# Performance work log

Hardware: AMD Instinct MI355X
Metric: run time of the kernel (lower is better)

Reference implementation:

```python
import jax, jax.numpy as jnp
import numpy as np

B, S, D = 1, 2048, 2048
H, HD = 16, 128  # n_heads, head_dim
ROPE_BASE = 100000.0


def setup_inputs() -> dict:
    key = jax.random.key(0)
    k0, k1, k2 = jax.random.split(key, 3)
    x = jax.random.normal(k0, (B, S, D), jnp.float32)
    # real RoPE table: (seq_len, head_dim//2, 2) holding (cos, sin)
    inv_freq = 1.0 / (ROPE_BASE ** (np.arange(0, HD, 2, dtype=np.float64) / HD))
    t = np.arange(S, dtype=np.float64)[:, None] * inv_freq[None, :]
    freqs_cis = jnp.asarray(np.stack([np.cos(t), np.sin(t)], axis=-1), jnp.float32)
    input_pos = jnp.arange(S, dtype=jnp.int32)
    Wqkv = jax.random.normal(k1, (D, 3 * D), jnp.float32) * (D ** -0.5)
    bqkv = jnp.zeros((3 * D,), jnp.float32)
    Wdense = jax.random.normal(k2, (D, D), jnp.float32) * (D ** -0.5)
    bdense = jnp.zeros((D,), jnp.float32)
    return {"x": x, "freqs_cis": freqs_cis, "input_pos": input_pos,
            "Wqkv": Wqkv, "bqkv": bqkv, "Wdense": Wdense, "bdense": bdense}


def apply_rotary_emb(x, freqs_cis):
    # x: [B, S, H, HD]; freqs_cis: [S, HD//2, 2]
    xs = x.reshape(*x.shape[:-1], -1, 2)  # [B,S,H,HD/2,2]
    fc = freqs_cis.reshape(1, xs.shape[1], 1, xs.shape[3], 2)
    out = jnp.stack([
        xs[..., 0] * fc[..., 0] - xs[..., 1] * fc[..., 1],
        xs[..., 1] * fc[..., 0] + xs[..., 0] * fc[..., 1],
    ], axis=-1)
    return out.reshape(x.shape).astype(x.dtype)


def reference(x, freqs_cis, input_pos, Wqkv, bqkv, Wdense, bdense):
    b, s, d = x.shape
    qkv = x @ Wqkv + bqkv                      # fused QKV projection
    q, k, v = jnp.split(qkv, 3, axis=-1)
    q = q.reshape(b, s, H, HD)
    k = k.reshape(b, s, H, HD)
    v = v.reshape(b, s, H, HD)
    q = apply_rotary_emb(q, freqs_cis)
    k = apply_rotary_emb(k, freqs_cis)
    # KV-cache update (cache batch = 1, max_seq = context_length)
    k_cache = jnp.zeros((1, S, H, HD), jnp.float32)
    v_cache = jnp.zeros((1, S, H, HD), jnp.float32)
    k_full = k_cache.at[:, input_pos].set(k)
    v_full = v_cache.at[:, input_pos].set(v)
    # causal SDPA in [B, H, S, HD] layout
    qh = q.transpose(0, 2, 1, 3)
    kh = k_full.transpose(0, 2, 1, 3)
    vh = v_full.transpose(0, 2, 1, 3)
    scale = HD ** -0.5
    scores = jnp.einsum('bhqd,bhkd->bhqk', qh, kh) * scale  # [B,H,S,S]
    causal = jnp.tril(jnp.ones((s, S), dtype=bool))
    scores = jnp.where(causal, scores, jnp.finfo(scores.dtype).min)
    attn = jax.nn.softmax(scores, axis=-1)
    ctx = jnp.einsum('bhqk,bhkd->bhqd', attn, vh)
    ctx = ctx.transpose(0, 2, 1, 3).reshape(b, s, d)
    return ctx @ Wdense + bdense
```

## Files before the change

kernel.cpp:

```cpp
#include <hip/hip_runtime.h>

#define S 2048
#define D 2048
#define H 16
#define HD 128
#define N3 6144

typedef __attribute__((ext_vector_type(8))) _Float16 f16x8;
typedef __attribute__((ext_vector_type(4))) float f32x4;
typedef unsigned short ushort_t;
typedef unsigned int uint_t;

__device__ __forceinline__ ushort_t f16_rne(float f) {
    _Float16 h = (_Float16)f;
    return __builtin_bit_cast(ushort_t, h);
}
__device__ __forceinline__ float f16_f32(ushort_t u) {
    return (float)__builtin_bit_cast(_Float16, u);
}

__global__ __launch_bounds__(256) void convert_f16_kernel(
    const float* __restrict__ in, ushort_t* __restrict__ hi)
{
    const int i = blockIdx.x * 256 + threadIdx.x;
    float4 v = ((const float4*)in)[i];
    ((ushort4*)hi)[i] = make_ushort4(f16_rne(v.x), f16_rne(v.y),
                                     f16_rne(v.z), f16_rne(v.w));
}

__global__ __launch_bounds__(256) void convert_t_kernel(
    const float* __restrict__ in, ushort_t* __restrict__ hi,
    int Kdim, int Ndim)
{
    __shared__ float tile[32][33];
    const int k0 = blockIdx.x * 32, n0 = blockIdx.y * 32;
    const int tx = threadIdx.x & 31, ty = threadIdx.x >> 5;
    #pragma unroll
    for (int r = 0; r < 4; r++)
        tile[ty + r * 8][tx] = in[(size_t)(k0 + ty + r * 8) * Ndim + n0 + tx];
    __syncthreads();
    const int n  = threadIdx.x >> 3;
    const int kc = (threadIdx.x & 7) * 4;
    const float v0 = tile[kc + 0][n], v1 = tile[kc + 1][n];
    const float v2 = tile[kc + 2][n], v3 = tile[kc + 3][n];
    const size_t off = (size_t)(n0 + n) * Kdim + k0 + kc;
    *(ushort4*)&hi[off] = make_ushort4(f16_rne(v0), f16_rne(v1),
                                       f16_rne(v2), f16_rne(v3));
}

__device__ __forceinline__ void gload16(const ushort_t* g, ushort_t* l) {
    __builtin_amdgcn_global_load_lds(
        (const __attribute__((address_space(1))) unsigned int*)g,
        (__attribute__((address_space(3))) unsigned int*)l, 16, 0, 0);
}

__device__ __forceinline__ void vwait8() { asm volatile("s_waitcnt vmcnt(8)" ::: "memory"); }
__device__ __forceinline__ void vwait4() { asm volatile("s_waitcnt vmcnt(4)" ::: "memory"); }
__device__ __forceinline__ void vwait0() { asm volatile("s_waitcnt vmcnt(0)" ::: "memory"); }
__device__ __forceinline__ void lwait0() { asm volatile("s_waitcnt lgkmcnt(0)" ::: "memory"); }

#define QNT 32

__device__ __forceinline__ void mm_core_8ph(
    const ushort_t* __restrict__ At, const ushort_t* __restrict__ Bt,
    ushort_t* lds, const int t, f32x4 (&acc)[4][4])
{
    const int w = t >> 6, lane = t & 63;
    const int lr = lane & 15, quad = lane >> 4;
    const int wm = (w & 1) * 64;
    const int wn = (w >> 1) * 64;

    const int srow = lane >> 2;
    const int scol = (lane & 3) * 8;
    const size_t goff0 = (size_t)(w * 16 + srow) * D + scol;
    const size_t goff1 = goff0 + (size_t)64 * D;
    const int ldst0 = w * 512;
    const int ldst1 = 2048 + w * 512;

    auto stage = [&](int j, int Tt) {
        const ushort_t* gb = (j & 1) ? Bt : At;
        const size_t off = (size_t)Tt * 64 + (j >> 1) * 32;
        ushort_t* dst = lds + (Tt & 1) * 16384 + j * 4096;
        gload16(gb + goff0 + off, dst + ldst0);
        gload16(gb + goff1 + off, dst + ldst1);
    };

    const int aro = (wm + lr) * 32 + quad * 8;
    const int bro = 4096 + (wn + lr) * 32 + quad * 8;

    stage(0, 0); stage(1, 0); stage(2, 0); stage(3, 0);
    stage(0, 1); stage(1, 1);
    vwait4();
    __builtin_amdgcn_sched_barrier(0);
    __builtin_amdgcn_s_barrier();

    f16x8 af[4], bf[4];

#define PH(kk, DOSTAGE, ST, WAITN)                                         \
    {                                                                      \
        const ushort_t* base = lds + (T & 1) * 16384 + (kk) * 8192;        \
        _Pragma("unroll")                                                  \
        for (int i = 0; i < 4; i++)                                        \
            af[i] = *(const f16x8*)&base[aro + i * 512];                   \
        _Pragma("unroll")                                                  \
        for (int n = 0; n < 4; n++)                                        \
            bf[n] = *(const f16x8*)&base[bro + n * 512];                   \
        if (DOSTAGE) {                                                     \
            stage((kk) ? 0 : 2, ST);                                       \
            stage((kk) ? 1 : 3, ST);                                       \
        }                                                                  \
        __builtin_amdgcn_s_barrier();                                      \
        lwait0();                                                          \
        __builtin_amdgcn_sched_barrier(0);                                 \
        __builtin_amdgcn_s_setprio(1);                                     \
        _Pragma("unroll")                                                  \
        for (int i = 0; i < 4; i++)                                        \
            _Pragma("unroll")                                              \
            for (int n = 0; n < 4; n++)                                    \
                acc[i][n] = __builtin_amdgcn_mfma_f32_16x16x32_f16(        \
                    af[i], bf[n], acc[i][n], 0, 0, 0);                     \
        __builtin_amdgcn_s_setprio(0);                                     \
        WAITN;                                                             \
        __builtin_amdgcn_s_barrier();                                      \
    }

    for (int T = 0; T < QNT - 2; T++) {
        PH(0, true, T + 1, vwait8());
        PH(1, true, T + 2, vwait8());
    }
    {
        const int T = QNT - 2;
        PH(0, true,  T + 1, vwait8());
        PH(1, false, 0,     vwait4());
    }
    {
        const int T = QNT - 1;
        PH(0, false, 0, vwait0());
        PH(1, false, 0, );
    }
#undef PH
}

__global__ __launch_bounds__(256, 2) void gemm_qkv_mfma(
    const ushort_t* __restrict__ xh,
    const ushort_t* __restrict__ Wth,
    const float* __restrict__ bias, const float* __restrict__ freqs,
    const int* __restrict__ input_pos,
    ushort_t* __restrict__ qhg, ushort_t* __restrict__ khg,
    ushort_t* __restrict__ vhg)
{
    __shared__ ushort_t lds[32768];
    const int t = threadIdx.x;
    const int col0 = blockIdx.x * 128;
    const int row0 = blockIdx.y * 128;

    f32x4 acc[4][4] = {};
    mm_core_8ph(xh + (size_t)row0 * D, Wth + (size_t)col0 * D, lds, t, acc);

    const int lane = t & 63;
    const int quad = lane >> 4;
    const int lr   = lane & 15;
    const int w = t >> 6;
    const int wm = (w & 1) * 64;
    const int wn = (w >> 1) * 64;

    const int which = col0 >> 11;
    const int hh = (col0 & 2047) >> 7;

    if (which == 2) {
        ushort_t* vh_b = vhg + (size_t)hh * HD * S;
        #pragma unroll
        for (int nt = 0; nt < 4; nt++) {
            const int d = wn + nt * 16 + lr;
            const float bsc = bias[col0 + d];
            #pragma unroll
            for (int mt = 0; mt < 4; mt++) {
                #pragma unroll
                for (int reg = 0; reg < 4; reg++) {
                    const int m = row0 + wm + mt * 16 + quad * 4 + reg;
                    const float v = acc[mt][nt][reg] + bsc;
                    vh_b[(size_t)d * S + input_pos[m]] = f16_rne(v);
                }
            }
        }
    } else {
        ushort_t* oh_b = ((which == 0) ? qhg : khg) + (size_t)hh * S * HD;
        #pragma unroll
        for (int nt = 0; nt < 4; nt++) {
            const int d = wn + nt * 16 + lr;
            const float bsc = bias[col0 + d];
            #pragma unroll
            for (int mt = 0; mt < 4; mt++) {
                #pragma unroll
                for (int reg = 0; reg < 4; reg++) {
                    const int m = row0 + wm + mt * 16 + quad * 4 + reg;
                    const float v = acc[mt][nt][reg] + bsc;
                    const float* fc = &freqs[((size_t)m * 64 + (d >> 1)) * 2];
                    const float cc = fc[0], ss = fc[1];
                    const float p = __shfl_xor(v, 1);
                    const float o = (d & 1) ? (v * cc + p * ss) : (v * cc - p * ss);
                    const ushort_t hv = f16_rne(o);
                    const int hp = __shfl_xor((int)hv, 1);
                    if (!(d & 1)) {
                        const int srowg = (which == 0) ? m : input_pos[m];
                        *(uint_t*)&oh_b[(size_t)srowg * HD + d] =
                            (uint_t)hv | ((uint_t)hp << 16);
                    }
                }
            }
        }
    }
}

__global__ __launch_bounds__(256, 2) void gemm_dense_mfma(
    const ushort_t* __restrict__ Ah,
    const ushort_t* __restrict__ Wth,
    const float* __restrict__ bias, float* __restrict__ out)
{
    __shared__ ushort_t lds[32768];
    const int t = threadIdx.x;
    const int col0 = blockIdx.x * 128;
    const int row0 = blockIdx.y * 128;

    f32x4 acc[4][4] = {};
    mm_core_8ph(Ah + (size_t)row0 * D, Wth + (size_t)col0 * D, lds, t, acc);

    const int lane = t & 63;
    const int quad = lane >> 4;
    const int lr   = lane & 15;
    const int w = t >> 6;
    const int wm = (w & 1) * 64;
    const int wn = (w >> 1) * 64;

    #pragma unroll
    for (int nt = 0; nt < 4; nt++) {
        const int n = col0 + wn + nt * 16 + lr;
        const float bsc = bias[n];
        #pragma unroll
        for (int mt = 0; mt < 4; mt++) {
            #pragma unroll
            for (int reg = 0; reg < 4; reg++) {
                const int m = row0 + wm + mt * 16 + quad * 4 + reg;
                const float o = acc[mt][nt][reg] + bsc;
                const float po = __shfl_xor(o, 1);
                if (!(n & 1))
                    *(float2*)&out[(size_t)m * D + n] = make_float2(o, po);
            }
        }
    }
}

__global__ __launch_bounds__(256, 2) void attn_mfma_kernel(
    const ushort_t* __restrict__ qhg, const ushort_t* __restrict__ khg,
    const ushort_t* __restrict__ vhg,
    float* __restrict__ Opart, float* __restrict__ MLpart)
{
    __shared__ ushort_t Khs[2][4096];
    __shared__ ushort_t Vhs[2][4096];
    __shared__ ushort_t Ps[64 * 32];

    const int bi   = blockIdx.x;
    const int h    = (bi & 7) + 8 * ((bi >> 3) & 1);
    const int half = (bi >> 4) & 1;
    const int qi   = bi >> 5;
    const int r = (h & 8) ? qi : (31 - qi);
    const int q0 = r * 64;
    const int nhalf = r + 1;
    const int kt0 = half * nhalf;
    const int kt1 = kt0 + nhalf;
    const int t = threadIdx.x;
    const int w = t >> 6, lane = t & 63;
    const int lr = lane & 15, quad = lane >> 4;

    const size_t qrow = (size_t)h * S + q0 + w * 16 + lr;
    f16x8 qf[4];
    #pragma unroll
    for (int ks = 0; ks < 4; ks++)
        qf[ks] = *(const f16x8*)&qhg[qrow * HD + ks * 32 + quad * 8];

    const ushort_t* kh_b = khg + (size_t)h * S * HD;
    const ushort_t* vh_b = vhg + (size_t)h * HD * S;

    const int keyq = lane >> 2;
    const int sub  = lane & 3;

    auto stage = [&](int kt, int buf) {
        const int k0 = kt * 32;
        #pragma unroll
        for (int hf = 0; hf < 2; hf++) {
            const size_t ksrc = (size_t)(k0 + hf * 16 + keyq) * HD + w * 32 + sub * 8;
            gload16(kh_b + ksrc, &Khs[buf][w * 1024 + hf * 512]);
            const int dim = w * 32 + hf * 16 + keyq;
            const size_t vsrc = (size_t)dim * S + k0 + sub * 8;
            gload16(vh_b + vsrc, &Vhs[buf][(w * 32 + hf * 16) * 32]);
        }
    };

    f32x4 O[8] = {};
    f32x4 Ol = {0.f, 0.f, 0.f, 0.f};
    float mrow[4];
    #pragma unroll
    for (int rr = 0; rr < 4; rr++) mrow[rr] = -1e30f;

    f16x8 onesv;
    #pragma unroll
    for (int i = 0; i < 8; i++) onesv[i] = (_Float16)1.0f;

    const float kSc = 0.08838834764831845f * 1.4426950408889634f;

    stage(kt0, 0);

    for (int kt = kt0; kt < kt1; kt++) {
        const int k0 = kt * 32;
        const int cur = (kt - kt0) & 1;
        __syncthreads();

        if (kt + 1 < kt1) stage(kt + 1, cur ^ 1);

        f32x4 sa[2];
        #pragma unroll
        for (int nt = 0; nt < 2; nt++) {
            f32x4 s = {0.f, 0.f, 0.f, 0.f};
            #pragma unroll
            for (int ks = 0; ks < 4; ks++) {
                f16x8 kf = *(const f16x8*)&Khs[cur][ks * 1024 + (nt * 16 + lr) * 32 + quad * 8];
                s = __builtin_amdgcn_mfma_f32_16x16x32_f16(qf[ks], kf, s, 0, 0, 0);
            }
            sa[nt] = s;
        }

        const int rowbase = q0 + w * 16 + quad * 4;
        const bool need_mask = (k0 + 31) > (q0 + w * 16);
        float alpha[4], pv0[4], pv1[4];
        #pragma unroll
        for (int rr = 0; rr < 4; rr++) {
            float z0 = sa[0][rr] * kSc;
            float z1 = sa[1][rr] * kSc;
            if (need_mask) {
                const int rowg = rowbase + rr;
                if (k0 + lr > rowg)      z0 = -1e30f;
                if (k0 + 16 + lr > rowg) z1 = -1e30f;
            }
            float rm = fmaxf(z0, z1);
            #pragma unroll
            for (int off = 1; off < 16; off <<= 1)
                rm = fmaxf(rm, __shfl_xor(rm, off));
            const float nm = fmaxf(mrow[rr], rm);
            alpha[rr] = exp2f(mrow[rr] - nm);
            pv0[rr] = exp2f(z0 - nm);
            pv1[rr] = exp2f(z1 - nm);
            mrow[rr] = nm;
        }

        #pragma unroll
        for (int rr = 0; rr < 4; rr++) {
            const int prow = (w * 16 + quad * 4 + rr) * 32;
            Ps[prow + lr]      = f16_rne(pv0[rr]);
            Ps[prow + 16 + lr] = f16_rne(pv1[rr]);
        }

        #pragma unroll
        for (int nt = 0; nt < 8; nt++)
            #pragma unroll
            for (int rr = 0; rr < 4; rr++)
                O[nt][rr] *= alpha[rr];
        #pragma unroll
        for (int rr = 0; rr < 4; rr++)
            Ol[rr] *= alpha[rr];
        const f16x8 pf = *(const f16x8*)&Ps[(w * 16 + lr) * 32 + quad * 8];
        #pragma unroll
        for (int nt = 0; nt < 8; nt++) {
            f16x8 vf = *(const f16x8*)&Vhs[cur][(nt * 16 + lr) * 32 + quad * 8];
            O[nt] = __builtin_amdgcn_mfma_f32_16x16x32_f16(pf, vf, O[nt], 0, 0, 0);
        }
        Ol = __builtin_amdgcn_mfma_f32_16x16x32_f16(pf, onesv, Ol, 0, 0, 0);
    }

    float* Ob = Opart + (size_t)bi * 64 * 128;
    #pragma unroll
    for (int rr = 0; rr < 4; rr++) {
        const int row = w * 16 + quad * 4 + rr;
        #pragma unroll
        for (int nt = 0; nt < 8; nt++)
            Ob[(size_t)row * 128 + nt * 16 + lr] = O[nt][rr];
        if (lr == 0) {
            MLpart[(size_t)bi * 128 + row * 2 + 0] = mrow[rr];
            MLpart[(size_t)bi * 128 + row * 2 + 1] = Ol[rr];
        }
    }
}

__global__ __launch_bounds__(128) void attn_combine_kernel(
    const float* __restrict__ Opart, const float* __restrict__ MLpart,
    ushort_t* __restrict__ ctxh)
{
    const int qt = blockIdx.x;
    const int h  = blockIdx.y;
    const int t  = threadIdx.x;
    const int b0 = h | (qt << 5);
    const int b1 = b0 | (1 << 4);
    const int r = (h & 8) ? qt : (31 - qt);
    const int q0 = r * 64;

    __shared__ float sc[64][2];
    if (t < 64) {
        const float m0 = MLpart[(size_t)b0 * 128 + t * 2 + 0];
        const float l0 = MLpart[(size_t)b0 * 128 + t * 2 + 1];
        const float m1 = MLpart[(size_t)b1 * 128 + t * 2 + 0];
        const float l1 = MLpart[(size_t)b1 * 128 + t * 2 + 1];
        const float m = fmaxf(m0, m1);
        const float a0 = exp2f(m0 - m), a1 = exp2f(m1 - m);
        const float inv = 1.0f / (l0 * a0 + l1 * a1);
        sc[t][0] = a0 * inv;
        sc[t][1] = a1 * inv;
    }
    __syncthreads();

    const float* O0 = Opart + (size_t)b0 * 64 * 128;
    const float* O1 = Opart + (size_t)b1 * 64 * 128;
    for (int row = 0; row < 64; row++) {
        const float o = O0[(size_t)row * 128 + t] * sc[row][0] +
                        O1[(size_t)row * 128 + t] * sc[row][1];
        ctxh[(size_t)(q0 + row) * D + h * HD + t] = f16_rne(o);
    }
}

__global__ __launch_bounds__(256) void gemm_qkv_kernel(
    const float* __restrict__ x, const float* __restrict__ W,
    const float* __restrict__ bias, const float* __restrict__ freqs,
    const int* __restrict__ input_pos,
    float* __restrict__ qb, float* __restrict__ kb, float* __restrict__ vb)
{
    __shared__ float As[16][68];
    __shared__ float Bs[16][64];
    const int bx = blockIdx.x;
    const int by = blockIdx.y;
    const int tid = threadIdx.x;
    const int tx = tid & 15, ty = tid >> 4;
    const int row0 = by * 64, col0 = bx * 64;
    const int am = tid >> 2;
    const int ak = (tid & 3) * 4;
    const int bk = tid >> 4;
    const int bn = (tid & 15) * 4;
    float acc[4][4] = {};
    for (int k0 = 0; k0 < D; k0 += 16) {
        float4 av = *(const float4*)&x[(size_t)(row0 + am) * D + k0 + ak];
        float4 bv = *(const float4*)&W[(size_t)(k0 + bk) * N3 + col0 + bn];
        __syncthreads();
        As[ak + 0][am] = av.x; As[ak + 1][am] = av.y;
        As[ak + 2][am] = av.z; As[ak + 3][am] = av.w;
        *(float4*)&Bs[bk][bn] = bv;
        __syncthreads();
        #pragma unroll
        for (int k = 0; k < 16; k++) {
            float4 a4 = *(const float4*)&As[k][ty * 4];
            float4 b4 = *(const float4*)&Bs[k][tx * 4];
            float a[4] = {a4.x, a4.y, a4.z, a4.w};
            float b[4] = {b4.x, b4.y, b4.z, b4.w};
            #pragma unroll
            for (int r = 0; r < 4; r++)
                #pragma unroll
                for (int c = 0; c < 4; c++)
                    acc[r][c] += a[r] * b[c];
        }
    }
    const int j0 = col0 + tx * 4;
    const int which = j0 >> 11;
    const int hh = (j0 & 2047) >> 7;
    const int d0 = j0 & 127;
    const float bv0 = bias[j0 + 0], bv1 = bias[j0 + 1];
    const float bv2 = bias[j0 + 2], bv3 = bias[j0 + 3];
    #pragma unroll
    for (int r = 0; r < 4; r++) {
        const int grow = row0 + ty * 4 + r;
        float v0 = acc[r][0] + bv0, v1 = acc[r][1] + bv1;
        float v2 = acc[r][2] + bv2, v3 = acc[r][3] + bv3;
        if (which == 2) {
            const int pos = input_pos[grow];
            float4 o4 = make_float4(v0, v1, v2, v3);
            *(float4*)&vb[((size_t)hh * S + pos) * HD + d0] = o4;
        } else {
            const float* fc = &freqs[((size_t)grow * 64 + (d0 >> 1)) * 2];
            float c0 = fc[0], s0 = fc[1], c1 = fc[2], s1 = fc[3];
            float o0 = v0 * c0 - v1 * s0, o1 = v1 * c0 + v0 * s0;
            float o2 = v2 * c1 - v3 * s1, o3 = v3 * c1 + v2 * s1;
            float4 o4 = make_float4(o0, o1, o2, o3);
            if (which == 0) {
                *(float4*)&qb[((size_t)hh * S + grow) * HD + d0] = o4;
            } else {
                const int pos = input_pos[grow];
                *(float4*)&kb[((size_t)hh * S + pos) * HD + d0] = o4;
            }
        }
    }
}

#define BQ 64
#define ABK 32
#define QSTR 132
#define KVSTR 132
#define PSTR 68

__global__ __launch_bounds__(256) void attn_kernel(
    const float* __restrict__ qb, const float* __restrict__ kb,
    const float* __restrict__ vb, float* __restrict__ ctx)
{
    __shared__ float Qs[BQ * QSTR];
    __shared__ float KV[ABK * KVSTR];
    __shared__ float Psf[ABK * PSTR];

    const int pa = blockIdx.x;
    const int h  = blockIdx.y;
    const int t  = threadIdx.x;
    const int ty = t >> 4, tx = t & 15;
    const int i0  = ty * 4;
    const int j0  = tx * 2;
    const int dd0 = tx * 8;
    const int lr = t >> 3;
    const int lc = (t & 7) * 4;

    const float* kbase = kb + (size_t)h * S * HD;
    const float* vbase = vb + (size_t)h * S * HD;
    const float kSc = 0.08838834764831845f * 1.4426950408889634f;

    for (int ph = 0; ph < 2; ph++) {
        const int r = (ph == 0) ? pa : 31 - pa;
        const int q0 = r * BQ;
        const int ntiles = 2 * r + 2;

        #pragma unroll
        for (int pp = 0; pp < 2; pp++) {
            const int iq = lr + pp * 32;
            const float* src = qb + ((size_t)h * S + q0 + iq) * HD;
            #pragma unroll
            for (int ch = 0; ch < 4; ch++)
                *(float4*)&Qs[iq * QSTR + lc + ch * 32] =
                    *(const float4*)&src[lc + ch * 32];
        }

        float O[4][8] = {};
        float m[4], l[4];
        #pragma unroll
        for (int rr = 0; rr < 4; rr++) { m[rr] = -1e30f; l[rr] = 0.f; }

        float4 kpref[4];
        #pragma unroll
        for (int ch = 0; ch < 4; ch++)
            kpref[ch] = *(const float4*)&kbase[(size_t)lr * HD + lc + ch * 32];

        __syncthreads();

        for (int kt = 0; kt < ntiles; kt++) {
            const int k0 = kt * ABK;

            #pragma unroll
            for (int ch = 0; ch < 4; ch++)
                *(float4*)&KV[lr * KVSTR + lc + ch * 32] = kpref[ch];
            __syncthreads();

            float4 vpref[4];
            #pragma unroll
            for (int ch = 0; ch < 4; ch++)
                vpref[ch] = *(const float4*)&vbase[(size_t)(k0 + lr) * HD + lc + ch * 32];

            float acc[4][2] = {};
            #pragma unroll 4
            for (int d0 = 0; d0 < HD; d0 += 4) {
                float4 ka = *(const float4*)&KV[(j0 + 0) * KVSTR + d0];
                float4 kb4 = *(const float4*)&KV[(j0 + 1) * KVSTR + d0];
                #pragma unroll
                for (int rr = 0; rr < 4; rr++) {
                    float4 q4 = *(const float4*)&Qs[(i0 + rr) * QSTR + d0];
                    acc[rr][0] += q4.x * ka.x + q4.y * ka.y + q4.z * ka.z + q4.w * ka.w;
                    acc[rr][1] += q4.x * kb4.x + q4.y * kb4.y + q4.z * kb4.z + q4.w * kb4.w;
                }
            }

            const bool need_mask = (k0 + ABK - 1) > q0;
            float p[4][2], alpha[4];
            #pragma unroll
            for (int rr = 0; rr < 4; rr++) {
                float z0 = acc[rr][0] * kSc;
                float z1 = acc[rr][1] * kSc;
                if (need_mask) {
                    if (k0 + j0 + 0 > q0 + i0 + rr) z0 = -1e30f;
                    if (k0 + j0 + 1 > q0 + i0 + rr) z1 = -1e30f;
                }
                float rmax = fmaxf(z0, z1);
                #pragma unroll
                for (int off = 1; off < 16; off <<= 1)
                    rmax = fmaxf(rmax, __shfl_xor(rmax, off, 16));
                const float nm = fmaxf(m[rr], rmax);
                alpha[rr] = exp2f(m[rr] - nm);
                p[rr][0] = exp2f(z0 - nm);
                p[rr][1] = exp2f(z1 - nm);
                float ts = p[rr][0] + p[rr][1];
                #pragma unroll
                for (int off = 1; off < 16; off <<= 1)
                    ts += __shfl_xor(ts, off, 16);
                l[rr] = l[rr] * alpha[rr] + ts;
                m[rr] = nm;
            }
            __syncthreads();

            #pragma unroll
            for (int ch = 0; ch < 4; ch++)
                *(float4*)&KV[lr * KVSTR + lc + ch * 32] = vpref[ch];
            *(float4*)&Psf[(j0 + 0) * PSTR + i0] =
                make_float4(p[0][0], p[1][0], p[2][0], p[3][0]);
            *(float4*)&Psf[(j0 + 1) * PSTR + i0] =
                make_float4(p[0][1], p[1][1], p[2][1], p[3][1]);
            if (kt + 1 < ntiles) {
                #pragma unroll
                for (int ch = 0; ch < 4; ch++)
                    kpref[ch] = *(const float4*)&kbase[(size_t)(k0 + ABK + lr) * HD + lc + ch * 32];
            }
            __syncthreads();

            #pragma unroll
            for (int rr = 0; rr < 4; rr++)
                #pragma unroll
                for (int c = 0; c < 8; c++)
                    O[rr][c] *= alpha[rr];
            #pragma unroll 4
            for (int j = 0; j < ABK; j++) {
                float4 pj = *(const float4*)&Psf[j * PSTR + i0];
                float4 v0 = *(const float4*)&KV[j * KVSTR + dd0];
                float4 v1 = *(const float4*)&KV[j * KVSTR + dd0 + 4];
                const float pr[4] = {pj.x, pj.y, pj.z, pj.w};
                const float vv[8] = {v0.x, v0.y, v0.z, v0.w, v1.x, v1.y, v1.z, v1.w};
                #pragma unroll
                for (int rr = 0; rr < 4; rr++)
                    #pragma unroll
                    for (int c = 0; c < 8; c++)
                        O[rr][c] += pr[rr] * vv[c];
            }
            __syncthreads();
        }

        #pragma unroll
        for (int rr = 0; rr < 4; rr++) {
            const float inv = 1.0f / l[rr];
            const int qg = q0 + i0 + rr;
            float4 o0 = make_float4(O[rr][0] * inv, O[rr][1] * inv,
                                    O[rr][2] * inv, O[rr][3] * inv);
            float4 o1 = make_float4(O[rr][4] * inv, O[rr][5] * inv,
                                    O[rr][6] * inv, O[rr][7] * inv);
            float* dst = &ctx[((size_t)qg * H + h) * HD + dd0];
            *(float4*)&dst[0] = o0;
            *(float4*)&dst[4] = o1;
        }
        __syncthreads();
    }
}

__global__ __launch_bounds__(256) void gemm_dense_kernel(
    const float* __restrict__ A, const float* __restrict__ W,
    const float* __restrict__ bias, float* __restrict__ out)
{
    __shared__ float As[16][68];
    __shared__ float Bs[16][64];
    const int bx = blockIdx.x;
    const int by = blockIdx.y;
    const int tid = threadIdx.x;
    const int tx = tid & 15, ty = tid >> 4;
    const int row0 = by * 64, col0 = bx * 64;
    const int am = tid >> 2;
    const int ak = (tid & 3) * 4;
    const int bk = tid >> 4;
    const int bn = (tid & 15) * 4;
    float acc[4][4] = {};
    for (int k0 = 0; k0 < D; k0 += 16) {
        float4 av = *(const float4*)&A[(size_t)(row0 + am) * D + k0 + ak];
        float4 bv = *(const float4*)&W[(size_t)(k0 + bk) * D + col0 + bn];
        __syncthreads();
        As[ak + 0][am] = av.x; As[ak + 1][am] = av.y;
        As[ak + 2][am] = av.z; As[ak + 3][am] = av.w;
        *(float4*)&Bs[bk][bn] = bv;
        __syncthreads();
        #pragma unroll
        for (int k = 0; k < 16; k++) {
            float4 a4 = *(const float4*)&As[k][ty * 4];
            float4 b4 = *(const float4*)&Bs[k][tx * 4];
            float a[4] = {a4.x, a4.y, a4.z, a4.w};
            float b[4] = {b4.x, b4.y, b4.z, b4.w};
            #pragma unroll
            for (int r = 0; r < 4; r++)
                #pragma unroll
                for (int c = 0; c < 4; c++)
                    acc[r][c] += a[r] * b[c];
        }
    }
    const int j0 = col0 + tx * 4;
    const float bv0 = bias[j0 + 0], bv1 = bias[j0 + 1];
    const float bv2 = bias[j0 + 2], bv3 = bias[j0 + 3];
    #pragma unroll
    for (int r = 0; r < 4; r++) {
        const int grow = row0 + ty * 4 + r;
        float4 o4 = make_float4(acc[r][0] + bv0, acc[r][1] + bv1,
                                acc[r][2] + bv2, acc[r][3] + bv3);
        *(float4*)&out[(size_t)grow * D + j0] = o4;
    }
}

extern "C" void kernel_launch(void* const* d_in, const int* in_sizes, int n_in,
                              void* d_out, int out_size, void* d_ws, size_t ws_size,
                              hipStream_t stream) {
    const float* x      = (const float*)d_in[0];
    const float* freqs  = (const float*)d_in[1];
    const int*   pos    = (const int*)d_in[2];
    const float* Wqkv   = (const float*)d_in[3];
    const float* bqkv   = (const float*)d_in[4];
    const float* Wdense = (const float*)d_in[5];
    const float* bdense = (const float*)d_in[6];
    float* out = (float*)d_out;

    const size_t nSD = (size_t)S * D;
    const size_t nW1 = (size_t)D * N3;
    const size_t nOP = (size_t)1024 * 64 * 128;
    const size_t nML = (size_t)1024 * 128;

    const size_t needed =
        (6 * nSD + nW1) * sizeof(ushort_t) + (nOP + nML) * sizeof(float);

    if (ws_size >= needed) {
        ushort_t* qh   = (ushort_t*)d_ws;
        ushort_t* kh   = qh + nSD;
        ushort_t* vh   = kh + nSD;
        ushort_t* ctxh = vh + nSD;
        ushort_t* xh   = ctxh + nSD;
        ushort_t* Wth  = xh + nSD;
        ushort_t* Wdth = Wth + nW1;
        float* Opart = (float*)(Wdth + nSD);
        float* MLpart = Opart + nOP;

        convert_f16_kernel<<<nSD / 4 / 256, 256, 0, stream>>>(x, xh);
        dim3 gt1(D / 32, N3 / 32);
        convert_t_kernel<<<gt1, 256, 0, stream>>>(Wqkv, Wth, D, N3);
        dim3 gt2(D / 32, D / 32);
        convert_t_kernel<<<gt2, 256, 0, stream>>>(Wdense, Wdth, D, D);

        dim3 g1(N3 / 128, S / 128);
        gemm_qkv_mfma<<<g1, 256, 0, stream>>>(xh, Wth, bqkv, freqs,
                                              pos, qh, kh, vh);
        attn_mfma_kernel<<<1024, 256, 0, stream>>>(qh, kh, vh,
                                                   Opart, MLpart);
        dim3 gc(32, H);
        attn_combine_kernel<<<gc, 128, 0, stream>>>(Opart, MLpart, ctxh);
        dim3 g3(D / 128, S / 128);
        gemm_dense_mfma<<<g3, 256, 0, stream>>>(ctxh, Wdth, bdense, out);
    } else {
        float* qb  = (float*)d_ws;
        float* kb  = qb + (size_t)H * S * HD;
        float* vb  = kb + (size_t)H * S * HD;
        float* ctx = vb + (size_t)H * S * HD;
        dim3 g1(N3 / 64, S / 64);
        gemm_qkv_kernel<<<g1, 256, 0, stream>>>(x, Wqkv, bqkv, freqs, pos, qb, kb, vb);
        dim3 g2(16, H);
        attn_kernel<<<g2, 256, 0, stream>>>(qb, kb, vb, ctx);
        dim3 g3(D / 64, S / 64);
        gemm_dense_kernel<<<g3, 256, 0, stream>>>(ctx, Wdense, bdense, out);
    }
}
```

Before: 340.7 us.

## Rework GEMM core to 8-wave blocks with XOR-swizzled LDS and unified K-tile staging

Replaces the 4-wave, 8-phase GEMM mainloop with an 8-wave (512-thread) version in which each wave computes a 64x32 sub-tile. A and B are staged for a full 64-wide K tile per step using an XOR-swizzled LDS layout, which is meant to avoid bank conflicts, and the stage is double-buffered with fewer barriers per iteration. The goal is higher occupancy and better latency hiding for the QKV and dense projections. Each wave now loads more LDS data per MFMA than before, and the launch bounds assume 4 blocks of 512 threads per CU, which adds register pressure.

```diff
diff --git a/kernel.cpp b/kernel.cpp
--- a/kernel.cpp
+++ b/kernel.cpp
@@ -54,94 +54,89 @@
         (__attribute__((address_space(3))) unsigned int*)l, 16, 0, 0);
 }
 
-__device__ __forceinline__ void vwait8() { asm volatile("s_waitcnt vmcnt(8)" ::: "memory"); }
 __device__ __forceinline__ void vwait4() { asm volatile("s_waitcnt vmcnt(4)" ::: "memory"); }
 __device__ __forceinline__ void vwait0() { asm volatile("s_waitcnt vmcnt(0)" ::: "memory"); }
 __device__ __forceinline__ void lwait0() { asm volatile("s_waitcnt lgkmcnt(0)" ::: "memory"); }
 
 #define QNT 32
 
-__device__ __forceinline__ void mm_core_8ph(
+__device__ __forceinline__ void mm_core_v4(
     const ushort_t* __restrict__ At, const ushort_t* __restrict__ Bt,
-    ushort_t* lds, const int t, f32x4 (&acc)[4][4])
+    ushort_t* lds, const int t, f32x4 (&acc)[4][2])
 {
     const int w = t >> 6, lane = t & 63;
     const int lr = lane & 15, quad = lane >> 4;
-    const int wm = (w & 1) * 64;
-    const int wn = (w >> 1) * 64;
-
-    const int srow = lane >> 2;
-    const int scol = (lane & 3) * 8;
-    const size_t goff0 = (size_t)(w * 16 + srow) * D + scol;
-    const size_t goff1 = goff0 + (size_t)64 * D;
-    const int ldst0 = w * 512;
-    const int ldst1 = 2048 + w * 512;
-
-    auto stage = [&](int j, int Tt) {
-        const ushort_t* gb = (j & 1) ? Bt : At;
-        const size_t off = (size_t)Tt * 64 + (j >> 1) * 32;
-        ushort_t* dst = lds + (Tt & 1) * 16384 + j * 4096;
-        gload16(gb + goff0 + off, dst + ldst0);
-        gload16(gb + goff1 + off, dst + ldst1);
+    const int wm = (w >> 2) * 64;
+    const int wn = (w & 3) * 32;
+
+    const int srow = w * 8 + (lane >> 3);
+    const int schk = ((lane & 7) ^ (lane >> 3)) * 8;
+    const int ldsw = w * 512;
+
+    auto stageAB = [&](int Tt) {
+        ushort_t* dbase = lds + (Tt & 1) * 16384;
+        const size_t koff = (size_t)Tt * 64 + schk;
+        gload16(At + (size_t)srow * D + koff,        dbase + ldsw);
+        gload16(At + (size_t)(srow + 64) * D + koff, dbase + 4096 + ldsw);
+        gload16(Bt + (size_t)srow * D + koff,        dbase + 8192 + ldsw);
+        gload16(Bt + (size_t)(srow + 64) * D + koff, dbase + 12288 + ldsw);
     };
 
-    const int aro = (wm + lr) * 32 + quad * 8;
-    const int bro = 4096 + (wn + lr) * 32 + quad * 8;
-
-    stage(0, 0); stage(1, 0); stage(2, 0); stage(3, 0);
-    stage(0, 1); stage(1, 1);
+    const int aoff = (wm + lr) * 64;
+    const int boff = 8192 + (wn + lr) * 64;
+    const int sw0 = ((0 * 4 + quad) ^ (lr & 7)) * 8;
+    const int sw1 = ((1 * 4 + quad) ^ (lr & 7)) * 8;
+
+    stageAB(0);
+    stageAB(1);
     vwait4();
     __builtin_amdgcn_sched_barrier(0);
     __builtin_amdgcn_s_barrier();
 
-    f16x8 af[4], bf[4];
-
-#define PH(kk, DOSTAGE, ST, WAITN)                                         \
-    {                                                                      \
-        const ushort_t* base = lds + (T & 1) * 16384 + (kk) * 8192;        \
-        _Pragma("unroll")                                                  \
-        for (int i = 0; i < 4; i++)                                        \
-            af[i] = *(const f16x8*)&base[aro + i * 512];                   \
-        _Pragma("unroll")                                                  \
-        for (int n = 0; n < 4; n++)                                        \
-            bf[n] = *(const f16x8*)&base[bro + n * 512];                   \
-        if (DOSTAGE) {                                                     \
-            stage((kk) ? 0 : 2, ST);                                       \
-            stage((kk) ? 1 : 3, ST);                                       \
-        }                                                                  \
-        __builtin_amdgcn_s_barrier();                                      \
-        lwait0();                                                          \
-        __builtin_amdgcn_sched_barrier(0);                                 \
-        __builtin_amdgcn_s_setprio(1);                                     \
-        _Pragma("unroll")                                                  \
-        for (int i = 0; i < 4; i++)                                        \
-            _Pragma("unroll")                                              \
-            for (int n = 0; n < 4; n++)                                    \
-                acc[i][n] = __builtin_amdgcn_mfma_f32_16x16x32_f16(        \
-                    af[i], bf[n], acc[i][n], 0, 0, 0);                     \
-        __builtin_amdgcn_s_setprio(0);                                     \
-        WAITN;                                                             \
-        __builtin_amdgcn_s_barrier();                                      \
-    }
-
-    for (int T = 0; T < QNT - 2; T++) {
-        PH(0, true, T + 1, vwait8());
-        PH(1, true, T + 2, vwait8());
-    }
-    {
-        const int T = QNT - 2;
-        PH(0, true,  T + 1, vwait8());
-        PH(1, false, 0,     vwait4());
-    }
-    {
-        const int T = QNT - 1;
-        PH(0, false, 0, vwait0());
-        PH(1, false, 0, );
-    }
-#undef PH
-}
-
-__global__ __launch_bounds__(256, 2) void gemm_qkv_mfma(
+    f16x8 a[4], b[2];
+    for (int T = 0; T < QNT; T++) {
+        const ushort_t* base = lds + (T & 1) * 16384;
+        #pragma unroll
+        for (int i = 0; i < 4; i++)
+            a[i] = *(const f16x8*)&base[aoff + i * 1024 + sw0];
+        #pragma unroll
+        for (int n = 0; n < 2; n++)
+            b[n] = *(const f16x8*)&base[boff + n * 1024 + sw0];
+        lwait0();
+        __builtin_amdgcn_sched_barrier(0);
+        __builtin_amdgcn_s_setprio(1);
+        #pragma unroll
+        for (int i = 0; i < 4; i++)
+            #pragma unroll
+            for (int n = 0; n < 2; n++)
+                acc[i][n] = __builtin_amdgcn_mfma_f32_16x16x32_f16(
+                    a[i], b[n], acc[i][n], 0, 0, 0);
+        __builtin_amdgcn_s_setprio(0);
+        #pragma unroll
+        for (int i = 0; i < 4; i++)
+            a[i] = *(const f16x8*)&base[aoff + i * 1024 + sw1];
+        #pragma unroll
+        for (int n = 0; n < 2; n++)
+            b[n] = *(const f16x8*)&base[boff + n * 1024 + sw1];
+        lwait0();
+        __builtin_amdgcn_sched_barrier(0);
+        __builtin_amdgcn_s_barrier();
+        if (T < QNT - 2) stageAB(T + 2);
+        __builtin_amdgcn_s_setprio(1);
+        #pragma unroll
+        for (int i = 0; i < 4; i++)
+            #pragma unroll
+            for (int n = 0; n < 2; n++)
+                acc[i][n] = __builtin_amdgcn_mfma_f32_16x16x32_f16(
+                    a[i], b[n], acc[i][n], 0, 0, 0);
+        __builtin_amdgcn_s_setprio(0);
+        if (T < QNT - 2)       vwait4();
+        else if (T == QNT - 2) vwait0();
+        __builtin_amdgcn_s_barrier();
+    }
+}
+
+__global__ __launch_bounds__(512, 4) void gemm_qkv_mfma(
     const ushort_t* __restrict__ xh,
     const ushort_t* __restrict__ Wth,
     const float* __restrict__ bias, const float* __restrict__ freqs,
@@ -154,15 +149,15 @@
     const int col0 = blockIdx.x * 128;
     const int row0 = blockIdx.y * 128;
 
-    f32x4 acc[4][4] = {};
-    mm_core_8ph(xh + (size_t)row0 * D, Wth + (size_t)col0 * D, lds, t, acc);
+    f32x4 acc[4][2] = {};
+    mm_core_v4(xh + (size_t)row0 * D, Wth + (size_t)col0 * D, lds, t, acc);
 
     const int lane = t & 63;
     const int quad = lane >> 4;
     const int lr   = lane & 15;
     const int w = t >> 6;
-    const int wm = (w & 1) * 64;
-    const int wn = (w >> 1) * 64;
+    const int wm = (w >> 2) * 64;
+    const int wn = (w & 3) * 32;
 
     const int which = col0 >> 11;
     const int hh = (col0 & 2047) >> 7;
@@ -170,7 +165,7 @@
     if (which == 2) {
         ushort_t* vh_b = vhg + (size_t)hh * HD * S;
         #pragma unroll
-        for (int nt = 0; nt < 4; nt++) {
+        for (int nt = 0; nt < 2; nt++) {
             const int d = wn + nt * 16 + lr;
             const float bsc = bias[col0 + d];
             #pragma unroll
@@ -186,7 +181,7 @@
     } else {
         ushort_t* oh_b = ((which == 0) ? qhg : khg) + (size_t)hh * S * HD;
         #pragma unroll
-        for (int nt = 0; nt < 4; nt++) {
+        for (int nt = 0; nt < 2; nt++) {
             const int d = wn + nt * 16 + lr;
             const float bsc = bias[col0 + d];
             #pragma unroll
@@ -212,7 +207,7 @@
     }
 }
 
-__global__ __launch_bounds__(256, 2) void gemm_dense_mfma(
+__global__ __launch_bounds__(512, 4) void gemm_dense_mfma(
     const ushort_t* __restrict__ Ah,
     const ushort_t* __restrict__ Wth,
     const float* __restrict__ bias, float* __restrict__ out)
@@ -222,18 +217,18 @@
     const int col0 = blockIdx.x * 128;
     const int row0 = blockIdx.y * 128;
 
-    f32x4 acc[4][4] = {};
-    mm_core_8ph(Ah + (size_t)row0 * D, Wth + (size_t)col0 * D, lds, t, acc);
+    f32x4 acc[4][2] = {};
+    mm_core_v4(Ah + (size_t)row0 * D, Wth + (size_t)col0 * D, lds, t, acc);
 
     const int lane = t & 63;
     const int quad = lane >> 4;
     const int lr   = lane & 15;
     const int w = t >> 6;
-    const int wm = (w & 1) * 64;
-    const int wn = (w >> 1) * 64;
+    const int wm = (w >> 2) * 64;
+    const int wn = (w & 3) * 32;
 
     #pragma unroll
-    for (int nt = 0; nt < 4; nt++) {
+    for (int nt = 0; nt < 2; nt++) {
         const int n = col0 + wn + nt * 16 + lr;
         const float bsc = bias[n];
         #pragma unroll
@@ -741,14 +736,14 @@
         convert_t_kernel<<<gt2, 256, 0, stream>>>(Wdense, Wdth, D, D);
 
         dim3 g1(N3 / 128, S / 128);
-        gemm_qkv_mfma<<<g1, 256, 0, stream>>>(xh, Wth, bqkv, freqs,
+        gemm_qkv_mfma<<<g1, 512, 0, stream>>>(xh, Wth, bqkv, freqs,
                                               pos, qh, kh, vh);
         attn_mfma_kernel<<<1024, 256, 0, stream>>>(qh, kh, vh,
                                                    Opart, MLpart);
         dim3 gc(32, H);
         attn_combine_kernel<<<gc, 128, 0, stream>>>(Opart, MLpart, ctxh);
         dim3 g3(D / 128, S / 128);
-        gemm_dense_mfma<<<g3, 256, 0, stream>>>(ctxh, Wdth, bdense, out);
+        gemm_dense_mfma<<<g3, 512, 0, stream>>>(ctxh, Wdth, bdense, out);
     } else {
         float* qb  = (float*)d_ws;
         float* kb  = qb + (size_t)H * S * HD;
```

Result: faster. 314.5 us (-7.7%).
